# Performance work log

Measured on AMD Instinct MI355X. Metric: run time of the kernel, lower is better.

## Reference

```python
import jax, jax.numpy as jnp
import numpy as np

B, S, E, H, I = 32, 257, 1024, 16, 4096
D = E // H  # head_dim = 64
EPS = 1e-5


def setup_inputs() -> dict:
    key = jax.random.key(0)
    ks = jax.random.split(key, 12)
    std = 0.02
    inp = {
        'hidden_states': jax.random.normal(ks[0], (B, S, E), jnp.float32),
        'attention_mask': jnp.zeros((B, 1, S, S), jnp.float32),
        'causal_attention_mask': jnp.zeros((B, 1, S, S), jnp.float32),
        'ln1_w': jnp.ones((E,), jnp.float32),
        'ln1_b': jnp.zeros((E,), jnp.float32),
        'q_w': jax.random.normal(ks[1], (E, E), jnp.float32) * std,
        'q_b': jnp.zeros((E,), jnp.float32),
        'k_w': jax.random.normal(ks[2], (E, E), jnp.float32) * std,
        'k_b': jnp.zeros((E,), jnp.float32),
        'v_w': jax.random.normal(ks[3], (E, E), jnp.float32) * std,
        'v_b': jnp.zeros((E,), jnp.float32),
        'o_w': jax.random.normal(ks[4], (E, E), jnp.float32) * std,
        'o_b': jnp.zeros((E,), jnp.float32),
        'ln2_w': jnp.ones((E,), jnp.float32),
        'ln2_b': jnp.zeros((E,), jnp.float32),
        'fc1_w': jax.random.normal(ks[5], (I, E), jnp.float32) * std,
        'fc1_b': jnp.zeros((I,), jnp.float32),
        'fc2_w': jax.random.normal(ks[6], (E, I), jnp.float32) * std,
        'fc2_b': jnp.zeros((E,), jnp.float32),
    }
    return inp


def _layernorm(x, w, b):
    mu = jnp.mean(x, axis=-1, keepdims=True)
    var = jnp.mean(jnp.square(x - mu), axis=-1, keepdims=True)
    return (x - mu) * jax.lax.rsqrt(var + EPS) * w + b


def _gelu_tanh(x):
    # 0.5*x*(1+tanh(sqrt(2/pi)*(x+0.044715*x^3)))
    c = np.sqrt(2.0 / np.pi).astype(np.float32)
    return 0.5 * x * (1.0 + jnp.tanh(c * (x + 0.044715 * x * x * x)))


def reference(hidden_states, attention_mask, causal_attention_mask,
              ln1_w, ln1_b, q_w, q_b, k_w, k_b, v_w, v_b, o_w, o_b,
              ln2_w, ln2_b, fc1_w, fc1_b, fc2_w, fc2_b):
    scale = D ** -0.5
    residual = hidden_states
    x = _layernorm(hidden_states, ln1_w, ln1_b)

    # projections (torch Linear: x @ W.T + b), q pre-scaled as in source
    q = (x @ q_w.T + q_b) * scale
    k = x @ k_w.T + k_b
    v = x @ v_w.T + v_b

    # [B, H, S, D]
    q = q.reshape(B, S, H, D).transpose(0, 2, 1, 3)
    k = k.reshape(B, S, H, D).transpose(0, 2, 1, 3)
    v = v.reshape(B, S, H, D).transpose(0, 2, 1, 3)

    scores = jnp.einsum('bhqd,bhkd->bhqk', q, k)  # [B,H,S,S]
    scores = scores + causal_attention_mask + attention_mask
    probs = jax.nn.softmax(scores, axis=-1)
    ctx = jnp.einsum('bhqk,bhkd->bhqd', probs, v)
    ctx = ctx.transpose(0, 2, 1, 3).reshape(B, S, E)
    attn_out = ctx @ o_w.T + o_b

    h = residual + attn_out
    residual = h
    x = _layernorm(h, ln2_w, ln2_b)
    x = _gelu_tanh(x @ fc1_w.T + fc1_b)
    x = x @ fc2_w.T + fc2_b
    return residual + x
```

## Files before the change

### kernel.cpp

```cpp
#include <hip/hip_runtime.h>

typedef unsigned short u16;
typedef unsigned int   u32;
typedef short s16x8 __attribute__((ext_vector_type(8)));
typedef float f32x4 __attribute__((ext_vector_type(4)));

#define MFMA16(A,B,C) __builtin_amdgcn_mfma_f32_16x16x32_bf16((A),(B),(C),0,0,0)
#define BAR()  asm volatile("s_barrier" ::: "memory")
#define VMC6   asm volatile("s_waitcnt vmcnt(6)" ::: "memory")
#define VMC0   asm volatile("s_waitcnt vmcnt(0)" ::: "memory")

#define B_   32
#define S_   257
#define E_   1024
#define H_   16
#define D_   64
#define I_   4096
#define M_   (B_*S_)
#define MT_  33

__device__ __forceinline__ u16 f2bf(float f) {
    u32 u = __float_as_uint(f);
    u32 r = u + 0x7fffu + ((u >> 16) & 1u);
    return (u16)(r >> 16);
}
__device__ __forceinline__ float bf2f(u16 b) {
    return __uint_as_float(((u32)b) << 16);
}

__device__ __forceinline__ void gload16(const void* g, void* l) {
    __builtin_amdgcn_global_load_lds(
        (const __attribute__((address_space(1))) u32*)g,
        (__attribute__((address_space(3))) u32*)l, 16, 0, 0);
}

__global__ __launch_bounds__(256)
void convert_w_kernel(const float* __restrict__ qw, const float* __restrict__ kw,
                      const float* __restrict__ vw, const float* __restrict__ ow,
                      const float* __restrict__ f1, const float* __restrict__ f2,
                      u16* __restrict__ dst)
{
    const int total4 = (12 * 1048576) / 4;
    for (int i = blockIdx.x * 256 + threadIdx.x; i < total4; i += gridDim.x * 256) {
        int e = i * 4;
        int seg = e >> 20;
        const float* srcp; int off;
        if (seg < 4)      { srcp = (seg == 0 ? qw : seg == 1 ? kw : seg == 2 ? vw : ow); off = e & 1048575; }
        else if (seg < 8) { srcp = f1; off = e - 4 * 1048576; }
        else              { srcp = f2; off = e - 8 * 1048576; }
        float4 v = *(const float4*)(srcp + off);
        ushort4 o;
        o.x = f2bf(v.x); o.y = f2bf(v.y); o.z = f2bf(v.z); o.w = f2bf(v.w);
        *(ushort4*)(dst + e) = o;
    }
}

__global__ __launch_bounds__(256)
void mask_combine_kernel(const float* __restrict__ am, const float* __restrict__ cm,
                         u16* __restrict__ msum)
{
    const int total = B_ * S_ * 272;
    for (int i = blockIdx.x * 256 + threadIdx.x; i < total; i += gridDim.x * 256) {
        int skv = i % 272;
        int rem = i / 272;
        int sq  = rem % S_;
        int b   = rem / S_;
        float v;
        if (skv < S_) {
            size_t o = ((size_t)b * S_ + sq) * S_ + skv;
            v = am[o] + cm[o];
        } else v = -1e30f;
        msum[i] = f2bf(v);
    }
}

__global__ __launch_bounds__(256)
void ln_kernel(const float* __restrict__ src, const float* __restrict__ gam,
               const float* __restrict__ bet, u16* __restrict__ dst)
{
    int row = blockIdx.x;
    const float4* p = (const float4*)(src + (size_t)row * E_);
    float4 x = p[threadIdx.x];
    float s  = x.x + x.y + x.z + x.w;
    float s2 = x.x * x.x + x.y * x.y + x.z * x.z + x.w * x.w;
#pragma unroll
    for (int xm = 1; xm < 64; xm <<= 1) {
        s  += __shfl_xor(s,  xm, 64);
        s2 += __shfl_xor(s2, xm, 64);
    }
    __shared__ float red[8];
    int wv = threadIdx.x >> 6;
    if ((threadIdx.x & 63) == 0) { red[wv] = s; red[4 + wv] = s2; }
    __syncthreads();
    s  = red[0] + red[1] + red[2] + red[3];
    s2 = red[4] + red[5] + red[6] + red[7];
    float mu  = s * (1.0f / 1024.0f);
    float var = s2 * (1.0f / 1024.0f) - mu * mu;
    float rs  = rsqrtf(var + 1e-5f);
    float4 g  = ((const float4*)gam)[threadIdx.x];
    float4 be = ((const float4*)bet)[threadIdx.x];
    ushort4 o;
    o.x = f2bf((x.x - mu) * rs * g.x + be.x);
    o.y = f2bf((x.y - mu) * rs * g.y + be.y);
    o.z = f2bf((x.z - mu) * rs * g.z + be.z);
    o.w = f2bf((x.w - mu) * rs * g.w + be.w);
    ((ushort4*)dst)[(size_t)row * 256 + threadIdx.x] = o;
}

template<int MODE>
__global__ __launch_bounds__(256, 2)
void gemmW(const u16* __restrict__ A,
           const u16* __restrict__ Bq, const u16* __restrict__ Bk, const u16* __restrict__ Bv,
           const float* __restrict__ biasq, const float* __restrict__ biask, const float* __restrict__ biasvv,
           const float* __restrict__ res, float* __restrict__ outF,
           u16* __restrict__ outBq, u16* __restrict__ outBk, u16* __restrict__ outBv,
           int M, int N, int K)
{
    __shared__ u16 lds[2][6][2048];
    const int tid = threadIdx.x, lane = tid & 63, w = tid >> 6;
    const int lr = lane & 15, lg = lane >> 4;
    const int wm = w >> 1, wn = w & 1;

    const int nwg = gridDim.x;
    const int q8 = nwg >> 3, r8 = nwg & 7;
    const int xcd = blockIdx.x & 7, o8 = blockIdx.x >> 3;
    int wg = (xcd < r8 ? xcd * (q8 + 1) : r8 * (q8 + 1) + (xcd - r8) * q8) + o8;

    const u16* Bm = Bq; const float* bias = biasq; u16* outB = outBq;
    float scl = 1.0f;
    const int NTL = N >> 7;
    if (MODE == 0) {
        int mat = wg / (MT_ * NTL); wg -= mat * (MT_ * NTL);
        if (mat == 1)      { Bm = Bk; bias = biask; outB = outBk; }
        else if (mat == 2) { Bm = Bv; bias = biasvv; outB = outBv; }
        if (mat == 0) scl = 0.125f;
    }
    const int mt = wg / NTL, nt = wg - mt * NTL;
    const int m0 = mt * 256, n0 = nt * 128;
    const int NTt = K >> 5;

    const int p    = tid * 16;
    const int l_   = p ^ (((p >> 7) & 3) << 4);
    const int srow = l_ >> 6;
    const int scol = (l_ & 63) >> 1;
    const int wbase = w * 1024;

    auto STAGE = [&](int buf, int t) {
        const int kc = t << 5;
#pragma unroll
        for (int s = 0; s < 4; ++s) {
            int gr = m0 + s * 64 + srow; if (gr > M - 1) gr = M - 1;
            gload16(A + (size_t)gr * K + kc + scol, (char*)&lds[buf][s][0] + wbase);
        }
#pragma unroll
        for (int s = 0; s < 2; ++s) {
            int gr = n0 + s * 64 + srow; if (gr > N - 1) gr = N - 1;
            gload16(Bm + (size_t)gr * K + kc + scol, (char*)&lds[buf][4 + s][0] + wbase);
        }
    };
    auto LDA = [&](int buf, int mf) -> s16x8 {
        int row = wm * 128 + mf * 16 + lr;
        const char* b = (const char*)&lds[buf][row >> 6][0];
        int ir = row & 63;
        return *(const s16x8*)(b + ir * 64 + ((lg * 16) ^ (((ir >> 1) & 3) << 4)));
    };
    auto LDB = [&](int buf, int nf) -> s16x8 {
        int row = wn * 64 + nf * 16 + lr;
        const char* b = (const char*)&lds[buf][4 + (row >> 6)][0];
        int ir = row & 63;
        return *(const s16x8*)(b + ir * 64 + ((lg * 16) ^ (((ir >> 1) & 3) << 4)));
    };

    f32x4 acc[8][4];
#pragma unroll
    for (int i = 0; i < 8; ++i)
#pragma unroll
        for (int j = 0; j < 4; ++j) { f32x4 z = {0.f, 0.f, 0.f, 0.f}; acc[i][j] = z; }

    STAGE(0, 0);
    STAGE(1, 1);
    VMC6;
    BAR();

    for (int t = 0; t < NTt; ++t) {
        const int cur = t & 1;
        s16x8 bf[4];
#pragma unroll
        for (int nf = 0; nf < 4; ++nf) bf[nf] = LDB(cur, nf);
#pragma unroll
        for (int mf = 0; mf < 8; ++mf) {
            s16x8 a = LDA(cur, mf);
#pragma unroll
            for (int nf = 0; nf < 4; ++nf)
                acc[mf][nf] = MFMA16(a, bf[nf], acc[mf][nf]);
        }
        BAR();
        if (t + 2 < NTt) STAGE(cur, t + 2);
        if (t + 1 < NTt) {
            if (t + 2 < NTt) { VMC6; } else { VMC0; }
        }
        BAR();
    }

    float biasv[4];
#pragma unroll
    for (int nf = 0; nf < 4; ++nf)
        biasv[nf] = bias[n0 + wn * 64 + nf * 16 + lr];

#pragma unroll
    for (int mf = 0; mf < 8; ++mf) {
#pragma unroll
        for (int r = 0; r < 4; ++r) {
            int row = m0 + wm * 128 + mf * 16 + lg * 4 + r;
            if (row >= M) continue;
            if (MODE == 0) {
                int bb = row / S_;
                int ss = row - bb * S_;
#pragma unroll
                for (int nf = 0; nf < 4; ++nf) {
                    int col = n0 + wn * 64 + nf * 16 + lr;
                    int hh = col >> 6, dd = col & 63;
                    float v = (acc[mf][nf][r] + biasv[nf]) * scl;
                    outB[(((size_t)bb * H_ + hh) * S_ + ss) * D_ + dd] = f2bf(v);
                }
            } else if (MODE == 1) {
                size_t base = (size_t)row * N;
#pragma unroll
                for (int nf = 0; nf < 4; ++nf) {
                    int col = n0 + wn * 64 + nf * 16 + lr;
                    outF[base + col] = acc[mf][nf][r] + biasv[nf] + res[base + col];
                }
            } else {
                size_t base = (size_t)row * N;
#pragma unroll
                for (int nf = 0; nf < 4; ++nf) {
                    int col = n0 + wn * 64 + nf * 16 + lr;
                    float x = acc[mf][nf][r] + biasv[nf];
                    float u2 = 1.5957691216057308f * (x + 0.044715f * x * x * x);
                    u2 = fminf(u2, 80.0f);
                    float tt = __expf(u2);
                    outB[base + col] = f2bf(x * tt / (1.0f + tt));
                }
            }
        }
    }
}

__global__ __launch_bounds__(256)
void attn_kernel(const u16* __restrict__ qg_, const u16* __restrict__ kg_,
                 const u16* __restrict__ vg_, const u16* __restrict__ msum,
                 u16* __restrict__ ctx)
{
    __shared__ u16 Ks[272 * 72];
    __shared__ u16 Vt[64 * 296];
    __shared__ u16 Ps[4][16 * 32];
    const int bh = blockIdx.x;
    const int b = bh >> 4, hh = bh & 15;
    const u16* kg = kg_ + (size_t)bh * (S_ * D_);
    const u16* vg = vg_ + (size_t)bh * (S_ * D_);
    const u16* qg = qg_ + (size_t)bh * (S_ * D_);
    const int tid = threadIdx.x, lane = tid & 63, wv = tid >> 6;

    for (int c = tid; c < (S_ * D_) / 8; c += 256) {
        int s = c >> 3, d8 = (c & 7) << 3;
        s16x8 val = *(const s16x8*)(kg + s * 64 + d8);
        *(s16x8*)&Ks[s * 72 + d8] = val;
    }
    for (int idx = tid; idx < 15 * 64; idx += 256) {
        int rr = 257 + (idx >> 6), cc = idx & 63;
        Ks[rr * 72 + cc] = 0;
    }
    for (int c = tid; c < (S_ * D_) / 8; c += 256) {
        int s = c >> 3, d8 = (c & 7) << 3;
        s16x8 val = *(const s16x8*)(vg + s * 64 + d8);
#pragma unroll
        for (int j = 0; j < 8; ++j) Vt[(d8 + j) * 296 + s] = (u16)val[j];
    }
    for (int idx = tid; idx < 64 * 39; idx += 256) {
        int dd = idx / 39, cc = 257 + idx % 39;
        Vt[dd * 296 + cc] = 0;
    }
    __syncthreads();

    const int lr = lane & 15, lg = lane >> 4;
    for (int qb = wv; qb < 17; qb += 4) {
        const int q0 = qb * 16;
        int qrow = q0 + lr; if (qrow > S_ - 1) qrow = S_ - 1;
        s16x8 aq0 = *(const s16x8*)(qg + qrow * 64 + lg * 8);
        s16x8 aq1 = *(const s16x8*)(qg + qrow * 64 + 32 + lg * 8);

        f32x4 sc[17];
#pragma unroll
        for (int t = 0; t < 17; ++t) { f32x4 z = {0.f, 0.f, 0.f, 0.f}; sc[t] = z; }
#pragma unroll
        for (int t = 0; t < 17; ++t) {
            s16x8 b0 = *(const s16x8*)&Ks[(t * 16 + lr) * 72 + lg * 8];
            s16x8 b1 = *(const s16x8*)&Ks[(t * 16 + lr) * 72 + 32 + lg * 8];
            sc[t] = MFMA16(aq0, b0, sc[t]);
            sc[t] = MFMA16(aq1, b1, sc[t]);
        }
        float mx[4] = {-3e38f, -3e38f, -3e38f, -3e38f};
#pragma unroll
        for (int r = 0; r < 4; ++r) {
            int sq = q0 + lg * 4 + r; if (sq > S_ - 1) sq = S_ - 1;
            const u16* mrow = msum + ((size_t)b * S_ + sq) * 272;
#pragma unroll
            for (int t = 0; t < 17; ++t) {
                sc[t][r] += bf2f(mrow[t * 16 + lr]);
                mx[r] = fmaxf(mx[r], sc[t][r]);
            }
        }
#pragma unroll
        for (int r = 0; r < 4; ++r) {
#pragma unroll
            for (int xm = 1; xm <= 8; xm <<= 1)
                mx[r] = fmaxf(mx[r], __shfl_xor(mx[r], xm, 64));
        }
        float sum[4] = {0.f, 0.f, 0.f, 0.f};
#pragma unroll
        for (int t = 0; t < 17; ++t)
#pragma unroll
            for (int r = 0; r < 4; ++r) {
                float e = __expf(sc[t][r] - mx[r]);
                sc[t][r] = e; sum[r] += e;
            }
#pragma unroll
        for (int r = 0; r < 4; ++r) {
#pragma unroll
            for (int xm = 1; xm <= 8; xm <<= 1)
                sum[r] += __shfl_xor(sum[r], xm, 64);
        }

        f32x4 ac[4];
#pragma unroll
        for (int nt = 0; nt < 4; ++nt) { f32x4 z = {0.f, 0.f, 0.f, 0.f}; ac[nt] = z; }
        u16* myP = &Ps[wv][0];
#pragma unroll
        for (int kc = 0; kc < 9; ++kc) {
#pragma unroll
            for (int tt = 0; tt < 2; ++tt) {
                const int t = kc * 2 + tt;
#pragma unroll
                for (int r = 0; r < 4; ++r) {
                    float pv = (t < 17) ? sc[(t < 17) ? t : 0][r] : 0.f;
                    myP[(lg * 4 + r) * 32 + tt * 16 + lr] = f2bf(pv);
                }
            }
            s16x8 pa = *(const s16x8*)&myP[lr * 32 + lg * 8];
#pragma unroll
            for (int nt = 0; nt < 4; ++nt) {
                s16x8 bv = *(const s16x8*)&Vt[(nt * 16 + lr) * 296 + kc * 32 + lg * 8];
                ac[nt] = MFMA16(pa, bv, ac[nt]);
            }
        }
#pragma unroll
        for (int r = 0; r < 4; ++r) {
            int sq = q0 + lg * 4 + r;
            if (sq < S_) {
                float rd = 1.0f / sum[r];
                size_t base = (((size_t)b * S_ + sq) * H_ + hh) * D_;
#pragma unroll
                for (int nt = 0; nt < 4; ++nt)
                    ctx[base + nt * 16 + lr] = f2bf(ac[nt][r] * rd);
            }
        }
    }
}

extern "C" void kernel_launch(void* const* d_in, const int* in_sizes, int n_in,
                              void* d_out, int out_size, void* d_ws, size_t ws_size,
                              hipStream_t stream)
{
    const float* hid   = (const float*)d_in[0];
    const float* am    = (const float*)d_in[1];
    const float* cm    = (const float*)d_in[2];
    const float* ln1w  = (const float*)d_in[3];
    const float* ln1b  = (const float*)d_in[4];
    const float* qw    = (const float*)d_in[5];
    const float* qbias = (const float*)d_in[6];
    const float* kw    = (const float*)d_in[7];
    const float* kbias = (const float*)d_in[8];
    const float* vw    = (const float*)d_in[9];
    const float* vbias = (const float*)d_in[10];
    const float* ow    = (const float*)d_in[11];
    const float* obias = (const float*)d_in[12];
    const float* ln2w  = (const float*)d_in[13];
    const float* ln2b  = (const float*)d_in[14];
    const float* f1w   = (const float*)d_in[15];
    const float* f1b   = (const float*)d_in[16];
    const float* f2w   = (const float*)d_in[17];
    const float* f2b   = (const float*)d_in[18];
    float* out = (float*)d_out;

    const size_t ME = (size_t)M_ * E_;
    u16* Wq   = (u16*)d_ws;
    u16* Wk   = Wq + 1048576;
    u16* Wv   = Wk + 1048576;
    u16* Wo   = Wv + 1048576;
    u16* Wf1  = Wo + 1048576;
    u16* Wf2  = Wf1 + 4 * 1048576;
    u16* xln  = Wf2 + 4 * 1048576;
    u16* qb_  = xln + ME;
    u16* kb_  = qb_ + ME;
    u16* vb_  = kb_ + ME;
    u16* ctx  = vb_ + ME;
    float* hbuf = (float*)(ctx + ME);
    u16* msum = (u16*)(hbuf + ME);
    u16* act  = qb_;
    u16* x2   = xln;

    convert_w_kernel<<<3072, 256, 0, stream>>>(qw, kw, vw, ow, f1w, f2w, Wq);
    mask_combine_kernel<<<8736, 256, 0, stream>>>(am, cm, msum);
    ln_kernel<<<M_, 256, 0, stream>>>(hid, ln1w, ln1b, xln);
    gemmW<0><<<3 * MT_ * 8, 256, 0, stream>>>(xln, Wq, Wk, Wv, qbias, kbias, vbias,
                                              nullptr, nullptr, qb_, kb_, vb_,
                                              M_, 1024, 1024);
    attn_kernel<<<512, 256, 0, stream>>>(qb_, kb_, vb_, msum, ctx);
    gemmW<1><<<MT_ * 8, 256, 0, stream>>>(ctx, Wo, nullptr, nullptr, obias, nullptr, nullptr,
                                          hid, hbuf, nullptr, nullptr, nullptr,
                                          M_, 1024, 1024);
    ln_kernel<<<M_, 256, 0, stream>>>(hbuf, ln2w, ln2b, x2);
    gemmW<2><<<MT_ * 32, 256, 0, stream>>>(x2, Wf1, nullptr, nullptr, f1b, nullptr, nullptr,
                                           nullptr, nullptr, act, nullptr, nullptr,
                                           M_, 4096, 1024);
    gemmW<1><<<MT_ * 8, 256, 0, stream>>>(act, Wf2, nullptr, nullptr, f2b, nullptr, nullptr,
                                          hbuf, out, nullptr, nullptr, nullptr,
                                          M_, 1024, 4096);
}
```

Before: 427.6 us.

## Make GEMM tile loop persistent and drop attention P buffer into K padding

Wraps the GEMM body in a grid-stride loop over output tiles so the grid can be smaller than the tile count. The FC1 GEMM is launched with 1024 blocks covering 1056 tiles, which puts its tail into a second pass. The attention kernel stops using its separate per-wave P scratch array and instead writes P into the unused padding columns of the K tile in LDS. It also adds a launch bound of 2 blocks per CU so that attention occupancy can rise. Every other grid size equals its tile count, so only FC1 changes scheduling, and that change may add tail imbalance.

```diff
diff --git a/kernel.cpp b/kernel.cpp
--- a/kernel.cpp
+++ b/kernel.cpp
@@ -114,29 +114,19 @@
            const float* __restrict__ biasq, const float* __restrict__ biask, const float* __restrict__ biasvv,
            const float* __restrict__ res, float* __restrict__ outF,
            u16* __restrict__ outBq, u16* __restrict__ outBk, u16* __restrict__ outBv,
-           int M, int N, int K)
+           int M, int N, int K, int ntiles)
 {
     __shared__ u16 lds[2][6][2048];
     const int tid = threadIdx.x, lane = tid & 63, w = tid >> 6;
     const int lr = lane & 15, lg = lane >> 4;
     const int wm = w >> 1, wn = w & 1;
 
-    const int nwg = gridDim.x;
-    const int q8 = nwg >> 3, r8 = nwg & 7;
+    const int G = gridDim.x;
+    const int q8 = G >> 3, r8 = G & 7;
     const int xcd = blockIdx.x & 7, o8 = blockIdx.x >> 3;
-    int wg = (xcd < r8 ? xcd * (q8 + 1) : r8 * (q8 + 1) + (xcd - r8) * q8) + o8;
-
-    const u16* Bm = Bq; const float* bias = biasq; u16* outB = outBq;
-    float scl = 1.0f;
+    const int wg0 = (xcd < r8 ? xcd * (q8 + 1) : r8 * (q8 + 1) + (xcd - r8) * q8) + o8;
+
     const int NTL = N >> 7;
-    if (MODE == 0) {
-        int mat = wg / (MT_ * NTL); wg -= mat * (MT_ * NTL);
-        if (mat == 1)      { Bm = Bk; bias = biask; outB = outBk; }
-        else if (mat == 2) { Bm = Bv; bias = biasvv; outB = outBv; }
-        if (mat == 0) scl = 0.125f;
-    }
-    const int mt = wg / NTL, nt = wg - mt * NTL;
-    const int m0 = mt * 256, n0 = nt * 128;
     const int NTt = K >> 5;
 
     const int p    = tid * 16;
@@ -145,115 +135,130 @@
     const int scol = (l_ & 63) >> 1;
     const int wbase = w * 1024;
 
-    auto STAGE = [&](int buf, int t) {
-        const int kc = t << 5;
-#pragma unroll
-        for (int s = 0; s < 4; ++s) {
-            int gr = m0 + s * 64 + srow; if (gr > M - 1) gr = M - 1;
-            gload16(A + (size_t)gr * K + kc + scol, (char*)&lds[buf][s][0] + wbase);
-        }
-#pragma unroll
-        for (int s = 0; s < 2; ++s) {
-            int gr = n0 + s * 64 + srow; if (gr > N - 1) gr = N - 1;
-            gload16(Bm + (size_t)gr * K + kc + scol, (char*)&lds[buf][4 + s][0] + wbase);
-        }
-    };
-    auto LDA = [&](int buf, int mf) -> s16x8 {
-        int row = wm * 128 + mf * 16 + lr;
-        const char* b = (const char*)&lds[buf][row >> 6][0];
-        int ir = row & 63;
-        return *(const s16x8*)(b + ir * 64 + ((lg * 16) ^ (((ir >> 1) & 3) << 4)));
-    };
-    auto LDB = [&](int buf, int nf) -> s16x8 {
-        int row = wn * 64 + nf * 16 + lr;
-        const char* b = (const char*)&lds[buf][4 + (row >> 6)][0];
-        int ir = row & 63;
-        return *(const s16x8*)(b + ir * 64 + ((lg * 16) ^ (((ir >> 1) & 3) << 4)));
-    };
-
-    f32x4 acc[8][4];
-#pragma unroll
-    for (int i = 0; i < 8; ++i)
-#pragma unroll
-        for (int j = 0; j < 4; ++j) { f32x4 z = {0.f, 0.f, 0.f, 0.f}; acc[i][j] = z; }
-
-    STAGE(0, 0);
-    STAGE(1, 1);
-    VMC6;
-    BAR();
-
-    for (int t = 0; t < NTt; ++t) {
-        const int cur = t & 1;
-        s16x8 bf[4];
-#pragma unroll
-        for (int nf = 0; nf < 4; ++nf) bf[nf] = LDB(cur, nf);
+    for (int tile = wg0; tile < ntiles; tile += G) {
+        int tw = tile;
+        const u16* Bm = Bq; const float* bias = biasq; u16* outB = outBq;
+        float scl = 1.0f;
+        if (MODE == 0) {
+            int mat = tw / (MT_ * NTL); tw -= mat * (MT_ * NTL);
+            if (mat == 1)      { Bm = Bk; bias = biask; outB = outBk; }
+            else if (mat == 2) { Bm = Bv; bias = biasvv; outB = outBv; }
+            else               { Bm = Bq; bias = biasq; outB = outBq; }
+            if (mat == 0) scl = 0.125f; else scl = 1.0f;
+        }
+        const int mt = tw / NTL, nt = tw - mt * NTL;
+        const int m0 = mt * 256, n0 = nt * 128;
+
+        auto STAGE = [&](int buf, int t) {
+            const int kc = t << 5;
+#pragma unroll
+            for (int s = 0; s < 4; ++s) {
+                int gr = m0 + s * 64 + srow; if (gr > M - 1) gr = M - 1;
+                gload16(A + (size_t)gr * K + kc + scol, (char*)&lds[buf][s][0] + wbase);
+            }
+#pragma unroll
+            for (int s = 0; s < 2; ++s) {
+                int gr = n0 + s * 64 + srow; if (gr > N - 1) gr = N - 1;
+                gload16(Bm + (size_t)gr * K + kc + scol, (char*)&lds[buf][4 + s][0] + wbase);
+            }
+        };
+        auto LDA = [&](int buf, int mf) -> s16x8 {
+            int row = wm * 128 + mf * 16 + lr;
+            const char* b = (const char*)&lds[buf][row >> 6][0];
+            int ir = row & 63;
+            return *(const s16x8*)(b + ir * 64 + ((lg * 16) ^ (((ir >> 1) & 3) << 4)));
+        };
+        auto LDB = [&](int buf, int nf) -> s16x8 {
+            int row = wn * 64 + nf * 16 + lr;
+            const char* b = (const char*)&lds[buf][4 + (row >> 6)][0];
+            int ir = row & 63;
+            return *(const s16x8*)(b + ir * 64 + ((lg * 16) ^ (((ir >> 1) & 3) << 4)));
+        };
+
+        f32x4 acc[8][4];
+#pragma unroll
+        for (int i = 0; i < 8; ++i)
+#pragma unroll
+            for (int j = 0; j < 4; ++j) { f32x4 z = {0.f, 0.f, 0.f, 0.f}; acc[i][j] = z; }
+
+        STAGE(0, 0);
+        STAGE(1, 1);
+        VMC6;
+        BAR();
+
+        for (int t = 0; t < NTt; ++t) {
+            const int cur = t & 1;
+            s16x8 bf[4];
+#pragma unroll
+            for (int nf = 0; nf < 4; ++nf) bf[nf] = LDB(cur, nf);
+#pragma unroll
+            for (int mf = 0; mf < 8; ++mf) {
+                s16x8 a = LDA(cur, mf);
+#pragma unroll
+                for (int nf = 0; nf < 4; ++nf)
+                    acc[mf][nf] = MFMA16(a, bf[nf], acc[mf][nf]);
+            }
+            BAR();
+            if (t + 2 < NTt) STAGE(cur, t + 2);
+            if (t + 1 < NTt) {
+                if (t + 2 < NTt) { VMC6; } else { VMC0; }
+            }
+            BAR();
+        }
+
+        float biasv[4];
+#pragma unroll
+        for (int nf = 0; nf < 4; ++nf)
+            biasv[nf] = bias[n0 + wn * 64 + nf * 16 + lr];
+
 #pragma unroll
         for (int mf = 0; mf < 8; ++mf) {
-            s16x8 a = LDA(cur, mf);
-#pragma unroll
-            for (int nf = 0; nf < 4; ++nf)
-                acc[mf][nf] = MFMA16(a, bf[nf], acc[mf][nf]);
-        }
-        BAR();
-        if (t + 2 < NTt) STAGE(cur, t + 2);
-        if (t + 1 < NTt) {
-            if (t + 2 < NTt) { VMC6; } else { VMC0; }
-        }
-        BAR();
-    }
-
-    float biasv[4];
-#pragma unroll
-    for (int nf = 0; nf < 4; ++nf)
-        biasv[nf] = bias[n0 + wn * 64 + nf * 16 + lr];
-
-#pragma unroll
-    for (int mf = 0; mf < 8; ++mf) {
-#pragma unroll
-        for (int r = 0; r < 4; ++r) {
-            int row = m0 + wm * 128 + mf * 16 + lg * 4 + r;
-            if (row >= M) continue;
-            if (MODE == 0) {
-                int bb = row / S_;
-                int ss = row - bb * S_;
-#pragma unroll
-                for (int nf = 0; nf < 4; ++nf) {
-                    int col = n0 + wn * 64 + nf * 16 + lr;
-                    int hh = col >> 6, dd = col & 63;
-                    float v = (acc[mf][nf][r] + biasv[nf]) * scl;
-                    outB[(((size_t)bb * H_ + hh) * S_ + ss) * D_ + dd] = f2bf(v);
+#pragma unroll
+            for (int r = 0; r < 4; ++r) {
+                int row = m0 + wm * 128 + mf * 16 + lg * 4 + r;
+                if (row >= M) continue;
+                if (MODE == 0) {
+                    int bb = row / S_;
+                    int ss = row - bb * S_;
+#pragma unroll
+                    for (int nf = 0; nf < 4; ++nf) {
+                        int col = n0 + wn * 64 + nf * 16 + lr;
+                        int hh = col >> 6, dd = col & 63;
+                        float v = (acc[mf][nf][r] + biasv[nf]) * scl;
+                        outB[(((size_t)bb * H_ + hh) * S_ + ss) * D_ + dd] = f2bf(v);
+                    }
+                } else if (MODE == 1) {
+                    size_t base = (size_t)row * N;
+#pragma unroll
+                    for (int nf = 0; nf < 4; ++nf) {
+                        int col = n0 + wn * 64 + nf * 16 + lr;
+                        outF[base + col] = acc[mf][nf][r] + biasv[nf] + res[base + col];
+                    }
+                } else {
+                    size_t base = (size_t)row * N;
+#pragma unroll
+                    for (int nf = 0; nf < 4; ++nf) {
+                        int col = n0 + wn * 64 + nf * 16 + lr;
+                        float x = acc[mf][nf][r] + biasv[nf];
+                        float u2 = 1.5957691216057308f * (x + 0.044715f * x * x * x);
+                        u2 = fminf(u2, 80.0f);
+                        float tt = __expf(u2);
+                        outB[base + col] = f2bf(x * tt / (1.0f + tt));
+                    }
                 }
-            } else if (MODE == 1) {
-                size_t base = (size_t)row * N;
-#pragma unroll
-                for (int nf = 0; nf < 4; ++nf) {
-                    int col = n0 + wn * 64 + nf * 16 + lr;
-                    outF[base + col] = acc[mf][nf][r] + biasv[nf] + res[base + col];
-                }
-            } else {
-                size_t base = (size_t)row * N;
-#pragma unroll
-                for (int nf = 0; nf < 4; ++nf) {
-                    int col = n0 + wn * 64 + nf * 16 + lr;
-                    float x = acc[mf][nf][r] + biasv[nf];
-                    float u2 = 1.5957691216057308f * (x + 0.044715f * x * x * x);
-                    u2 = fminf(u2, 80.0f);
-                    float tt = __expf(u2);
-                    outB[base + col] = f2bf(x * tt / (1.0f + tt));
-                }
-            }
-        }
-    }
-}
-
-__global__ __launch_bounds__(256)
+            }
+        }
+        if (tile + G < ntiles) BAR();
+    }
+}
+
+__global__ __launch_bounds__(256, 2)
 void attn_kernel(const u16* __restrict__ qg_, const u16* __restrict__ kg_,
                  const u16* __restrict__ vg_, const u16* __restrict__ msum,
                  u16* __restrict__ ctx)
 {
     __shared__ u16 Ks[272 * 72];
     __shared__ u16 Vt[64 * 296];
-    __shared__ u16 Ps[4][16 * 32];
     const int bh = blockIdx.x;
     const int b = bh >> 4, hh = bh & 15;
     const u16* kg = kg_ + (size_t)bh * (S_ * D_);
@@ -334,7 +339,7 @@
         f32x4 ac[4];
 #pragma unroll
         for (int nt = 0; nt < 4; ++nt) { f32x4 z = {0.f, 0.f, 0.f, 0.f}; ac[nt] = z; }
-        u16* myP = &Ps[wv][0];
+        u16* pbase = &Ks[(size_t)wv * 64 * 72];
 #pragma unroll
         for (int kc = 0; kc < 9; ++kc) {
 #pragma unroll
@@ -343,10 +348,11 @@
 #pragma unroll
                 for (int r = 0; r < 4; ++r) {
                     float pv = (t < 17) ? sc[(t < 17) ? t : 0][r] : 0.f;
-                    myP[(lg * 4 + r) * 32 + tt * 16 + lr] = f2bf(pv);
+                    int pr = lg * 4 + r, pc = tt * 16 + lr;
+                    pbase[(pr * 4 + (pc >> 3)) * 72 + 64 + (pc & 7)] = f2bf(pv);
                 }
             }
-            s16x8 pa = *(const s16x8*)&myP[lr * 32 + lg * 8];
+            s16x8 pa = *(const s16x8*)&pbase[(lr * 4 + lg) * 72 + 64];
 #pragma unroll
             for (int nt = 0; nt < 4; ++nt) {
                 s16x8 bv = *(const s16x8*)&Vt[(nt * 16 + lr) * 296 + kc * 32 + lg * 8];
@@ -412,18 +418,18 @@
     convert_w_kernel<<<3072, 256, 0, stream>>>(qw, kw, vw, ow, f1w, f2w, Wq);
     mask_combine_kernel<<<8736, 256, 0, stream>>>(am, cm, msum);
     ln_kernel<<<M_, 256, 0, stream>>>(hid, ln1w, ln1b, xln);
-    gemmW<0><<<3 * MT_ * 8, 256, 0, stream>>>(xln, Wq, Wk, Wv, qbias, kbias, vbias,
-                                              nullptr, nullptr, qb_, kb_, vb_,
-                                              M_, 1024, 1024);
+    gemmW<0><<<792, 256, 0, stream>>>(xln, Wq, Wk, Wv, qbias, kbias, vbias,
+                                      nullptr, nullptr, qb_, kb_, vb_,
+                                      M_, 1024, 1024, 792);
     attn_kernel<<<512, 256, 0, stream>>>(qb_, kb_, vb_, msum, ctx);
-    gemmW<1><<<MT_ * 8, 256, 0, stream>>>(ctx, Wo, nullptr, nullptr, obias, nullptr, nullptr,
-                                          hid, hbuf, nullptr, nullptr, nullptr,
-                                          M_, 1024, 1024);
+    gemmW<1><<<264, 256, 0, stream>>>(ctx, Wo, nullptr, nullptr, obias, nullptr, nullptr,
+                                      hid, hbuf, nullptr, nullptr, nullptr,
+                                      M_, 1024, 1024, 264);
     ln_kernel<<<M_, 256, 0, stream>>>(hbuf, ln2w, ln2b, x2);
-    gemmW<2><<<MT_ * 32, 256, 0, stream>>>(x2, Wf1, nullptr, nullptr, f1b, nullptr, nullptr,
-                                           nullptr, nullptr, act, nullptr, nullptr,
-                                           M_, 4096, 1024);
-    gemmW<1><<<MT_ * 8, 256, 0, stream>>>(act, Wf2, nullptr, nullptr, f2b, nullptr, nullptr,
-                                          hbuf, out, nullptr, nullptr, nullptr,
-                                          M_, 1024, 4096);
-}
+    gemmW<2><<<1024, 256, 0, stream>>>(x2, Wf1, nullptr, nullptr, f1b, nullptr, nullptr,
+                                       nullptr, nullptr, act, nullptr, nullptr,
+                                       M_, 4096, 1024, 1056);
+    gemmW<1><<<264, 256, 0, stream>>>(act, Wf2, nullptr, nullptr, f2b, nullptr, nullptr,
+                                      hbuf, out, nullptr, nullptr, nullptr,
+                                      M_, 1024, 4096, 264);
+}
```

Result: no change. 425.0 us (-0.6%).

## Add producer-wave warp-specialized GEMM with triple-buffered LDS and smaller tiles

Applied to the files above, without the earlier changes.

Replaces the 256x128 double-buffered GEMM with a 320-thread kernel. A dedicated fifth wave issues all global-to-LDS loads into a 3-stage ring, while four compute waves do MFMA on 128x128 tiles, synchronised only by barriers. This is meant to overlap memory loads with compute and to raise occupancy through smaller per-block LDS and register use. The attention kernel also drops its separate P scratch buffer, reusing padding columns of the K tile in LDS so two blocks can fit per CU. The risks are more barrier traffic, smaller tiles that reuse less data, and the XCD mapping now assuming the grid size is a multiple of 8.

```diff
diff --git a/kernel.cpp b/kernel.cpp
--- a/kernel.cpp
+++ b/kernel.cpp
@@ -6,9 +6,9 @@
 typedef float f32x4 __attribute__((ext_vector_type(4)));
 
 #define MFMA16(A,B,C) __builtin_amdgcn_mfma_f32_16x16x32_bf16((A),(B),(C),0,0,0)
-#define BAR()  asm volatile("s_barrier" ::: "memory")
-#define VMC6   asm volatile("s_waitcnt vmcnt(6)" ::: "memory")
-#define VMC0   asm volatile("s_waitcnt vmcnt(0)" ::: "memory")
+#define BAR()   asm volatile("s_barrier" ::: "memory")
+#define VMC16   asm volatile("s_waitcnt vmcnt(16)" ::: "memory")
+#define VMC0    asm volatile("s_waitcnt vmcnt(0)" ::: "memory")
 
 #define B_   32
 #define S_   257
@@ -17,7 +17,7 @@
 #define D_   64
 #define I_   4096
 #define M_   (B_*S_)
-#define MT_  33
+#define MT2_ 65
 
 __device__ __forceinline__ u16 f2bf(float f) {
     u32 u = __float_as_uint(f);
@@ -108,97 +108,105 @@
 }
 
 template<int MODE>
-__global__ __launch_bounds__(256, 2)
-void gemmW(const u16* __restrict__ A,
+__global__ __launch_bounds__(320, 3)
+void gemmP(const u16* __restrict__ A,
            const u16* __restrict__ Bq, const u16* __restrict__ Bk, const u16* __restrict__ Bv,
            const float* __restrict__ biasq, const float* __restrict__ biask, const float* __restrict__ biasvv,
            const float* __restrict__ res, float* __restrict__ outF,
            u16* __restrict__ outBq, u16* __restrict__ outBk, u16* __restrict__ outBv,
            int M, int N, int K)
 {
-    __shared__ u16 lds[2][6][2048];
+    __shared__ u16 lds[3][4][2048];
     const int tid = threadIdx.x, lane = tid & 63, w = tid >> 6;
     const int lr = lane & 15, lg = lane >> 4;
     const int wm = w >> 1, wn = w & 1;
 
-    const int nwg = gridDim.x;
-    const int q8 = nwg >> 3, r8 = nwg & 7;
+    const int G = gridDim.x;
+    const int q8 = G >> 3;
     const int xcd = blockIdx.x & 7, o8 = blockIdx.x >> 3;
-    int wg = (xcd < r8 ? xcd * (q8 + 1) : r8 * (q8 + 1) + (xcd - r8) * q8) + o8;
+    int wg = xcd * q8 + o8;
 
     const u16* Bm = Bq; const float* bias = biasq; u16* outB = outBq;
     float scl = 1.0f;
     const int NTL = N >> 7;
     if (MODE == 0) {
-        int mat = wg / (MT_ * NTL); wg -= mat * (MT_ * NTL);
+        int mat = wg / (MT2_ * NTL); wg -= mat * (MT2_ * NTL);
         if (mat == 1)      { Bm = Bk; bias = biask; outB = outBk; }
         else if (mat == 2) { Bm = Bv; bias = biasvv; outB = outBv; }
         if (mat == 0) scl = 0.125f;
     }
     const int mt = wg / NTL, nt = wg - mt * NTL;
-    const int m0 = mt * 256, n0 = nt * 128;
+    const int m0 = mt * 128, n0 = nt * 128;
     const int NTt = K >> 5;
 
-    const int p    = tid * 16;
-    const int l_   = p ^ (((p >> 7) & 3) << 4);
-    const int srow = l_ >> 6;
-    const int scol = (l_ & 63) >> 1;
-    const int wbase = w * 1024;
-
-    auto STAGE = [&](int buf, int t) {
-        const int kc = t << 5;
-#pragma unroll
-        for (int s = 0; s < 4; ++s) {
-            int gr = m0 + s * 64 + srow; if (gr > M - 1) gr = M - 1;
-            gload16(A + (size_t)gr * K + kc + scol, (char*)&lds[buf][s][0] + wbase);
-        }
-#pragma unroll
-        for (int s = 0; s < 2; ++s) {
-            int gr = n0 + s * 64 + srow; if (gr > N - 1) gr = N - 1;
-            gload16(Bm + (size_t)gr * K + kc + scol, (char*)&lds[buf][4 + s][0] + wbase);
-        }
-    };
+    if (w == 4) {
+        const int lp = lane * 16;
+        auto PSTAGE = [&](int buf, int t) {
+            const int kc = t << 5;
+#pragma unroll
+            for (int s = 0; s < 4; ++s) {
+                const u16* src = (s < 2) ? A : Bm;
+                const int g0   = (s < 2) ? (m0 + (s & 1) * 64) : (n0 + (s & 1) * 64);
+                const int gmax = (s < 2) ? (M - 1) : (N - 1);
+#pragma unroll
+                for (int c = 0; c < 4; ++c) {
+                    int p  = c * 1024 + lp;
+                    int l_ = p ^ (((p >> 7) & 3) << 4);
+                    int srow = l_ >> 6, scol = (l_ & 63) >> 1;
+                    int gr = g0 + srow; if (gr > gmax) gr = gmax;
+                    gload16(src + (size_t)gr * K + kc + scol,
+                            (char*)&lds[buf][s][0] + p);
+                }
+            }
+        };
+        PSTAGE(0, 0);
+        PSTAGE(1, 1);
+        VMC16;
+        BAR();
+        for (int t = 0; t < NTt; ++t) {
+            if (t + 2 < NTt) {
+                PSTAGE((t + 2) % 3, t + 2);
+                if (t + 1 < NTt) VMC16;
+            } else if (t + 1 < NTt) {
+                VMC0;
+            }
+            BAR();
+        }
+        return;
+    }
+
     auto LDA = [&](int buf, int mf) -> s16x8 {
-        int row = wm * 128 + mf * 16 + lr;
+        int row = wm * 64 + mf * 16 + lr;
         const char* b = (const char*)&lds[buf][row >> 6][0];
         int ir = row & 63;
         return *(const s16x8*)(b + ir * 64 + ((lg * 16) ^ (((ir >> 1) & 3) << 4)));
     };
     auto LDB = [&](int buf, int nf) -> s16x8 {
         int row = wn * 64 + nf * 16 + lr;
-        const char* b = (const char*)&lds[buf][4 + (row >> 6)][0];
+        const char* b = (const char*)&lds[buf][2 + (row >> 6)][0];
         int ir = row & 63;
         return *(const s16x8*)(b + ir * 64 + ((lg * 16) ^ (((ir >> 1) & 3) << 4)));
     };
 
-    f32x4 acc[8][4];
-#pragma unroll
-    for (int i = 0; i < 8; ++i)
+    f32x4 acc[4][4];
+#pragma unroll
+    for (int i = 0; i < 4; ++i)
 #pragma unroll
         for (int j = 0; j < 4; ++j) { f32x4 z = {0.f, 0.f, 0.f, 0.f}; acc[i][j] = z; }
 
-    STAGE(0, 0);
-    STAGE(1, 1);
-    VMC6;
     BAR();
-
     for (int t = 0; t < NTt; ++t) {
-        const int cur = t & 1;
-        s16x8 bf[4];
+        const int cur = t % 3;
+        s16x8 bf[4], af[4];
 #pragma unroll
         for (int nf = 0; nf < 4; ++nf) bf[nf] = LDB(cur, nf);
 #pragma unroll
-        for (int mf = 0; mf < 8; ++mf) {
-            s16x8 a = LDA(cur, mf);
+        for (int mf = 0; mf < 4; ++mf) af[mf] = LDA(cur, mf);
+#pragma unroll
+        for (int mf = 0; mf < 4; ++mf)
 #pragma unroll
             for (int nf = 0; nf < 4; ++nf)
-                acc[mf][nf] = MFMA16(a, bf[nf], acc[mf][nf]);
-        }
-        BAR();
-        if (t + 2 < NTt) STAGE(cur, t + 2);
-        if (t + 1 < NTt) {
-            if (t + 2 < NTt) { VMC6; } else { VMC0; }
-        }
+                acc[mf][nf] = MFMA16(af[mf], bf[nf], acc[mf][nf]);
         BAR();
     }
 
@@ -208,10 +216,10 @@
         biasv[nf] = bias[n0 + wn * 64 + nf * 16 + lr];
 
 #pragma unroll
-    for (int mf = 0; mf < 8; ++mf) {
+    for (int mf = 0; mf < 4; ++mf) {
 #pragma unroll
         for (int r = 0; r < 4; ++r) {
-            int row = m0 + wm * 128 + mf * 16 + lg * 4 + r;
+            int row = m0 + wm * 64 + mf * 16 + lg * 4 + r;
             if (row >= M) continue;
             if (MODE == 0) {
                 int bb = row / S_;
@@ -246,14 +254,13 @@
     }
 }
 
-__global__ __launch_bounds__(256)
+__global__ __launch_bounds__(256, 2)
 void attn_kernel(const u16* __restrict__ qg_, const u16* __restrict__ kg_,
                  const u16* __restrict__ vg_, const u16* __restrict__ msum,
                  u16* __restrict__ ctx)
 {
     __shared__ u16 Ks[272 * 72];
     __shared__ u16 Vt[64 * 296];
-    __shared__ u16 Ps[4][16 * 32];
     const int bh = blockIdx.x;
     const int b = bh >> 4, hh = bh & 15;
     const u16* kg = kg_ + (size_t)bh * (S_ * D_);
@@ -334,7 +341,7 @@
         f32x4 ac[4];
 #pragma unroll
         for (int nt = 0; nt < 4; ++nt) { f32x4 z = {0.f, 0.f, 0.f, 0.f}; ac[nt] = z; }
-        u16* myP = &Ps[wv][0];
+        u16* pbase = &Ks[(size_t)wv * 64 * 72];
 #pragma unroll
         for (int kc = 0; kc < 9; ++kc) {
 #pragma unroll
@@ -343,10 +350,11 @@
 #pragma unroll
                 for (int r = 0; r < 4; ++r) {
                     float pv = (t < 17) ? sc[(t < 17) ? t : 0][r] : 0.f;
-                    myP[(lg * 4 + r) * 32 + tt * 16 + lr] = f2bf(pv);
+                    int pr = lg * 4 + r, pc = tt * 16 + lr;
+                    pbase[(pr * 4 + (pc >> 3)) * 72 + 64 + (pc & 7)] = f2bf(pv);
                 }
             }
-            s16x8 pa = *(const s16x8*)&myP[lr * 32 + lg * 8];
+            s16x8 pa = *(const s16x8*)&pbase[(lr * 4 + lg) * 72 + 64];
 #pragma unroll
             for (int nt = 0; nt < 4; ++nt) {
                 s16x8 bv = *(const s16x8*)&Vt[(nt * 16 + lr) * 296 + kc * 32 + lg * 8];
@@ -412,18 +420,18 @@
     convert_w_kernel<<<3072, 256, 0, stream>>>(qw, kw, vw, ow, f1w, f2w, Wq);
     mask_combine_kernel<<<8736, 256, 0, stream>>>(am, cm, msum);
     ln_kernel<<<M_, 256, 0, stream>>>(hid, ln1w, ln1b, xln);
-    gemmW<0><<<3 * MT_ * 8, 256, 0, stream>>>(xln, Wq, Wk, Wv, qbias, kbias, vbias,
-                                              nullptr, nullptr, qb_, kb_, vb_,
-                                              M_, 1024, 1024);
+    gemmP<0><<<3 * MT2_ * 8, 320, 0, stream>>>(xln, Wq, Wk, Wv, qbias, kbias, vbias,
+                                               nullptr, nullptr, qb_, kb_, vb_,
+                                               M_, 1024, 1024);
     attn_kernel<<<512, 256, 0, stream>>>(qb_, kb_, vb_, msum, ctx);
-    gemmW<1><<<MT_ * 8, 256, 0, stream>>>(ctx, Wo, nullptr, nullptr, obias, nullptr, nullptr,
-                                          hid, hbuf, nullptr, nullptr, nullptr,
-                                          M_, 1024, 1024);
+    gemmP<1><<<MT2_ * 8, 320, 0, stream>>>(ctx, Wo, nullptr, nullptr, obias, nullptr, nullptr,
+                                           hid, hbuf, nullptr, nullptr, nullptr,
+                                           M_, 1024, 1024);
     ln_kernel<<<M_, 256, 0, stream>>>(hbuf, ln2w, ln2b, x2);
-    gemmW<2><<<MT_ * 32, 256, 0, stream>>>(x2, Wf1, nullptr, nullptr, f1b, nullptr, nullptr,
-                                           nullptr, nullptr, act, nullptr, nullptr,
-                                           M_, 4096, 1024);
-    gemmW<1><<<MT_ * 8, 256, 0, stream>>>(act, Wf2, nullptr, nullptr, f2b, nullptr, nullptr,
-                                          hbuf, out, nullptr, nullptr, nullptr,
-                                          M_, 1024, 4096);
-}
+    gemmP<2><<<MT2_ * 32, 320, 0, stream>>>(x2, Wf1, nullptr, nullptr, f1b, nullptr, nullptr,
+                                            nullptr, nullptr, act, nullptr, nullptr,
+                                            M_, 4096, 1024);
+    gemmP<1><<<MT2_ * 8, 320, 0, stream>>>(act, Wf2, nullptr, nullptr, f2b, nullptr, nullptr,
+                                           hbuf, out, nullptr, nullptr, nullptr,
+                                           M_, 1024, 4096);
+}
```

After: 464.0 us. +8.5%, slower.
